# Kernel optimization log

Hardware: AMD Instinct MI355X
Metric: run time of the kernel (lower is better)

The kernel has to match this reference:

```python
import jax, jax.numpy as jnp
import numpy as np

NEG_INF = -1e30

def setup_inputs() -> dict:
    key0 = jax.random.key(0)
    kq, kk, kv, ks = jax.random.split(key0, 4)
    B, S, H, D = 4, 2048, 16, 128
    query = jax.random.normal(kq, (B, S, H, D), dtype=jnp.float32)
    key = jax.random.normal(kk, (B, S, H, D), dtype=jnp.float32)
    value = jax.random.normal(kv, (B, S, H, D), dtype=jnp.float32)
    decoder_segment_ids = jnp.sort(jax.random.randint(ks, (B, S), 0, 4), axis=-1).astype(jnp.int32)
    return {"query": query, "key": key, "value": value,
            "decoder_segment_ids": decoder_segment_ids}

def reference(query, key, value, decoder_segment_ids):
    # Splash causal attention, no 1/sqrt(d) scale (matches the wrapped kernel).
    B, S, H, D = query.shape
    # scores: [b, h, q, k]
    scores = jnp.einsum('bqhd,bkhd->bhqk', query, key)
    causal = jnp.tril(jnp.ones((S, S), dtype=bool))              # [q, k]
    seg = decoder_segment_ids
    seg_mask = seg[:, :, None] == seg[:, None, :]                # [b, q, k]
    mask = causal[None, None, :, :] & seg_mask[:, None, :, :]    # [b, 1->h, q, k]
    scores = jnp.where(mask, scores, NEG_INF)
    probs = jax.nn.softmax(scores, axis=-1)
    out = jnp.einsum('bhqk,bkhd->bqhd', probs, value)
    return out
```

## Files before the change

kernel.cpp:

```cpp
#include <hip/hip_runtime.h>
#include <hip/hip_bf16.h>

typedef short v8s __attribute__((ext_vector_type(8)));
typedef float f32x4 __attribute__((ext_vector_type(4)));

constexpr int Bb = 4, S = 2048, H = 16, Dd = 128;
constexpr int BQ = 64, BK = 32;
constexpr float NEG = -1e30f;

static __device__ inline short f2bs(float x) {
    __hip_bfloat16 h = __float2bfloat16(x);
    return *reinterpret_cast<short*>(&h);
}
static __device__ inline float bs2f(short s) {
    unsigned u = ((unsigned)(unsigned short)s) << 16;
    return __uint_as_float(u);
}

__global__ __launch_bounds__(256) void fa_fwd(const float* __restrict__ q,
                                              const float* __restrict__ k,
                                              const float* __restrict__ v,
                                              const int* __restrict__ seg,
                                              float* __restrict__ out) {
    __shared__ __align__(16) short Kh[BK][136];
    __shared__ __align__(16) short Kl[BK][136];
    __shared__ __align__(16) short Vt[Dd][40];
    __shared__ __align__(16) short Pl[4][16][40];

    const int qt = blockIdx.x, h = blockIdx.y, b = blockIdx.z;
    const int q0 = qt * BQ;
    const int tid = threadIdx.x;
    const int wave = tid >> 6, lane = tid & 63;
    const int quad = lane >> 4, l16 = lane & 15;

    const int rowA = q0 + wave * 16 + l16;
    const float* qbase = q + (((size_t)b * S + rowA) * H + h) * Dd;
    v8s qh[4], qlo[4];
#pragma unroll
    for (int c = 0; c < 4; ++c) {
        f32x4 x0 = *(const f32x4*)(qbase + c * 32 + quad * 8);
        f32x4 x1 = *(const f32x4*)(qbase + c * 32 + quad * 8 + 4);
#pragma unroll
        for (int i = 0; i < 4; ++i) {
            short h0 = f2bs(x0[i]); qh[c][i]     = h0; qlo[c][i]     = f2bs(x0[i] - bs2f(h0));
            short h1 = f2bs(x1[i]); qh[c][4 + i] = h1; qlo[c][4 + i] = f2bs(x1[i] - bs2f(h1));
        }
    }

    const int rowC0 = q0 + wave * 16 + quad * 4;
    int segq[4];
#pragma unroll
    for (int r = 0; r < 4; ++r) segq[r] = seg[b * S + rowC0 + r];
    const int seg_lo = seg[b * S + q0];

    f32x4 o[8];
#pragma unroll
    for (int dt = 0; dt < 8; ++dt) o[dt] = f32x4{0.f, 0.f, 0.f, 0.f};
    float m_i[4], l_i[4];
#pragma unroll
    for (int r = 0; r < 4; ++r) { m_i[r] = NEG; l_i[r] = 0.f; }

    const int nkt = (q0 + BQ) / BK;
    for (int it = 0; it < nkt; ++it) {
        const int kt = it * BK;
        if (seg[b * S + kt + BK - 1] < seg_lo) continue;

        {
            const int kk = tid >> 3, d0 = (tid & 7) * 16;
            const float* kb = k + (((size_t)b * S + kt + kk) * H + h) * Dd + d0;
            const float* vb = v + (((size_t)b * S + kt + kk) * H + h) * Dd + d0;
#pragma unroll
            for (int j = 0; j < 4; ++j) {
                f32x4 x = *(const f32x4*)(kb + j * 4);
#pragma unroll
                for (int i = 0; i < 4; ++i) {
                    short hb = f2bs(x[i]);
                    Kh[kk][d0 + j * 4 + i] = hb;
                    Kl[kk][d0 + j * 4 + i] = f2bs(x[i] - bs2f(hb));
                }
                f32x4 y = *(const f32x4*)(vb + j * 4);
#pragma unroll
                for (int i = 0; i < 4; ++i) Vt[d0 + j * 4 + i][kk] = f2bs(y[i]);
            }
        }
        __syncthreads();

        float sc[2][4];
#pragma unroll
        for (int nt = 0; nt < 2; ++nt) {
            f32x4 s = f32x4{0.f, 0.f, 0.f, 0.f};
#pragma unroll
            for (int c = 0; c < 4; ++c) {
                v8s kfh = *(const v8s*)&Kh[nt * 16 + l16][c * 32 + quad * 8];
                v8s kfl = *(const v8s*)&Kl[nt * 16 + l16][c * 32 + quad * 8];
                s = __builtin_amdgcn_mfma_f32_16x16x32_bf16(qh[c], kfh, s, 0, 0, 0);
                s = __builtin_amdgcn_mfma_f32_16x16x32_bf16(qlo[c], kfh, s, 0, 0, 0);
                s = __builtin_amdgcn_mfma_f32_16x16x32_bf16(qh[c], kfl, s, 0, 0, 0);
            }
            const int kj = kt + nt * 16 + l16;
            const int segk = seg[b * S + kj];
#pragma unroll
            for (int r = 0; r < 4; ++r) {
                const int qi = rowC0 + r;
                const bool valid = (kj <= qi) && (segk == segq[r]);
                sc[nt][r] = valid ? s[r] : NEG;
            }
        }

        float pr[2][4];
#pragma unroll
        for (int r = 0; r < 4; ++r) {
            float mx = fmaxf(sc[0][r], sc[1][r]);
#pragma unroll
            for (int off = 1; off < 16; off <<= 1) mx = fmaxf(mx, __shfl_xor(mx, off));
            const float mn = fmaxf(m_i[r], mx);
            const float alpha = __expf(m_i[r] - mn);
            const float p0 = (sc[0][r] <= 0.5f * NEG) ? 0.f : __expf(sc[0][r] - mn);
            const float p1 = (sc[1][r] <= 0.5f * NEG) ? 0.f : __expf(sc[1][r] - mn);
            float rs = p0 + p1;
#pragma unroll
            for (int off = 1; off < 16; off <<= 1) rs += __shfl_xor(rs, off);
            l_i[r] = l_i[r] * alpha + rs;
            m_i[r] = mn;
#pragma unroll
            for (int dt = 0; dt < 8; ++dt) o[dt][r] *= alpha;
            pr[0][r] = p0;
            pr[1][r] = p1;
        }

#pragma unroll
        for (int nt = 0; nt < 2; ++nt)
#pragma unroll
            for (int r = 0; r < 4; ++r)
                Pl[wave][quad * 4 + r][nt * 16 + l16] = f2bs(pr[nt][r]);
        __syncthreads();

        v8s pf = *(const v8s*)&Pl[wave][l16][quad * 8];
#pragma unroll
        for (int dt = 0; dt < 8; ++dt) {
            v8s vf = *(const v8s*)&Vt[dt * 16 + l16][quad * 8];
            o[dt] = __builtin_amdgcn_mfma_f32_16x16x32_bf16(pf, vf, o[dt], 0, 0, 0);
        }
        __syncthreads();
    }

    const size_t obase = (((size_t)b * S + rowC0) * H + h) * Dd;
#pragma unroll
    for (int r = 0; r < 4; ++r) {
        const float inv = 1.0f / l_i[r];
#pragma unroll
        for (int dt = 0; dt < 8; ++dt)
            out[obase + (size_t)r * H * Dd + dt * 16 + l16] = o[dt][r] * inv;
    }
}

extern "C" void kernel_launch(void* const* d_in, const int* in_sizes, int n_in,
                              void* d_out, int out_size, void* d_ws, size_t ws_size,
                              hipStream_t stream) {
    const float* q = (const float*)d_in[0];
    const float* k = (const float*)d_in[1];
    const float* v = (const float*)d_in[2];
    const int* seg = (const int*)d_in[3];
    float* out = (float*)d_out;
    dim3 grid(S / BQ, H, Bb);
    fa_fwd<<<grid, dim3(256), 0, stream>>>(q, k, v, seg, out);
}
```

Baseline: 403.9 us.

## Precompute bf16 hi/lo K and transposed V in workspace, prefetch tiles in register

Adds pre-pass kernels that split K into bf16 hi/lo halves and write a transposed bf16 V into workspace. The attention kernel then loads ready-made bf16 tiles with vector loads and register-prefetches the next non-skipped tile while computing the current one. It also drops a barrier between the per-wave P write and read. This removes repeated fp32 conversion and V transposition per query tile, at the cost of extra passes writing the converted K and V to memory. It falls back to the old kernel if the workspace is too small.

```diff
diff --git a/kernel.cpp b/kernel.cpp
--- a/kernel.cpp
+++ b/kernel.cpp
@@ -7,6 +7,7 @@
 constexpr int Bb = 4, S = 2048, H = 16, Dd = 128;
 constexpr int BQ = 64, BK = 32;
 constexpr float NEG = -1e30f;
+constexpr size_t NELEM = (size_t)Bb * S * H * Dd;
 
 static __device__ inline short f2bs(float x) {
     __hip_bfloat16 h = __float2bfloat16(x);
@@ -17,22 +18,212 @@
     return __uint_as_float(u);
 }
 
-__global__ __launch_bounds__(256) void fa_fwd(const float* __restrict__ q,
-                                              const float* __restrict__ k,
-                                              const float* __restrict__ v,
-                                              const int* __restrict__ seg,
-                                              float* __restrict__ out) {
+__global__ __launch_bounds__(256) void prep_k(const float* __restrict__ k,
+                                              short* __restrict__ khi,
+                                              short* __restrict__ klo) {
+    size_t i = ((size_t)blockIdx.x * 256 + threadIdx.x) * 8;
+    f32x4 a = *(const f32x4*)(k + i);
+    f32x4 b = *(const f32x4*)(k + i + 4);
+    v8s hi, lo;
+#pragma unroll
+    for (int j = 0; j < 4; ++j) {
+        short h0 = f2bs(a[j]); hi[j] = h0;     lo[j] = f2bs(a[j] - bs2f(h0));
+        short h1 = f2bs(b[j]); hi[4 + j] = h1; lo[4 + j] = f2bs(b[j] - bs2f(h1));
+    }
+    *(v8s*)(khi + i) = hi;
+    *(v8s*)(klo + i) = lo;
+}
+
+__global__ __launch_bounds__(256) void prep_vt(const float* __restrict__ v,
+                                               short* __restrict__ vt) {
+    __shared__ __align__(16) short T[64][136];
+    const int k0 = blockIdx.x * 64, h = blockIdx.y, b = blockIdx.z;
+    const int t = threadIdx.x;
+    {
+        const int kk = t >> 2, c0 = (t & 3) * 32;
+        const float* vb = v + (((size_t)b * S + k0 + kk) * H + h) * Dd + c0;
+        short tmp[32];
+#pragma unroll
+        for (int j = 0; j < 32; j += 4) {
+            f32x4 x = *(const f32x4*)(vb + j);
+#pragma unroll
+            for (int i = 0; i < 4; ++i) tmp[j + i] = f2bs(x[i]);
+        }
+#pragma unroll
+        for (int j = 0; j < 4; ++j) *(v8s*)&T[kk][c0 + j * 8] = *(v8s*)&tmp[j * 8];
+    }
+    __syncthreads();
+    {
+        const int d = t >> 1, koff = (t & 1) * 32;
+        short o16[32];
+#pragma unroll
+        for (int i = 0; i < 32; ++i) o16[i] = T[koff + i][d];
+        short* dst = vt + ((size_t)(b * H + h) * Dd + d) * S + k0 + koff;
+#pragma unroll
+        for (int j = 0; j < 4; ++j) *(v8s*)(dst + j * 8) = *(v8s*)&o16[j * 8];
+    }
+}
+
+__global__ __launch_bounds__(256) void fa_fast(const short* __restrict__ khi,
+                                               const short* __restrict__ klo,
+                                               const short* __restrict__ vtg,
+                                               const float* __restrict__ q,
+                                               const int* __restrict__ seg,
+                                               float* __restrict__ out) {
+    __shared__ __align__(16) short Khl[BK][136];
+    __shared__ __align__(16) short Kll[BK][136];
+    __shared__ __align__(16) short Vtl[Dd][40];
+    __shared__ __align__(16) short Pl[4][16][40];
+
+    const int qt = blockIdx.x, h = blockIdx.y, b = blockIdx.z;
+    const int q0 = qt * BQ, tid = threadIdx.x;
+    const int wave = tid >> 6, lane = tid & 63;
+    const int quad = lane >> 4, l16 = lane & 15;
+
+    const int rowA = q0 + wave * 16 + l16;
+    const float* qbase = q + (((size_t)b * S + rowA) * H + h) * Dd;
+    v8s qh[4], ql[4];
+#pragma unroll
+    for (int c = 0; c < 4; ++c) {
+        f32x4 x0 = *(const f32x4*)(qbase + c * 32 + quad * 8);
+        f32x4 x1 = *(const f32x4*)(qbase + c * 32 + quad * 8 + 4);
+#pragma unroll
+        for (int i = 0; i < 4; ++i) {
+            short h0 = f2bs(x0[i]); qh[c][i] = h0;     ql[c][i] = f2bs(x0[i] - bs2f(h0));
+            short h1 = f2bs(x1[i]); qh[c][4 + i] = h1; ql[c][4 + i] = f2bs(x1[i] - bs2f(h1));
+        }
+    }
+
+    const int rowC0 = q0 + wave * 16 + quad * 4;
+    const int segb = b * S;
+    int segq[4];
+#pragma unroll
+    for (int r = 0; r < 4; ++r) segq[r] = seg[segb + rowC0 + r];
+    const int seg_lo = seg[segb + q0];
+
+    f32x4 o[8];
+#pragma unroll
+    for (int dt = 0; dt < 8; ++dt) o[dt] = f32x4{0.f, 0.f, 0.f, 0.f};
+    float m_i[4], l_i[4];
+#pragma unroll
+    for (int r = 0; r < 4; ++r) { m_i[r] = NEG; l_i[r] = 0.f; }
+
+    const int skk = tid >> 3, scol = (tid & 7) * 16;
+    const int svd = tid >> 1, svo = (tid & 1) * 16;
+    const size_t kbase = (((size_t)b * S + skk) * H + h) * Dd + scol;
+    const size_t vbase = ((size_t)(b * H + h) * Dd + svd) * S + svo;
+
+    const int nkt = (q0 + BQ) / BK;
+    int it = 0;
+    while (it < nkt && seg[segb + it * BK + BK - 1] < seg_lo) ++it;
+
+    v8s pA, pB, pC, pD, pE, pF;
+    if (it < nkt) {
+        const size_t ka = kbase + (size_t)it * BK * H * Dd;
+        pA = *(const v8s*)(khi + ka); pB = *(const v8s*)(khi + ka + 8);
+        pC = *(const v8s*)(klo + ka); pD = *(const v8s*)(klo + ka + 8);
+        const size_t va = vbase + (size_t)it * BK;
+        pE = *(const v8s*)(vtg + va); pF = *(const v8s*)(vtg + va + 8);
+    }
+
+    while (it < nkt) {
+        *(v8s*)&Khl[skk][scol] = pA; *(v8s*)&Khl[skk][scol + 8] = pB;
+        *(v8s*)&Kll[skk][scol] = pC; *(v8s*)&Kll[skk][scol + 8] = pD;
+        *(v8s*)&Vtl[svd][svo]  = pE; *(v8s*)&Vtl[svd][svo + 8]  = pF;
+        __syncthreads();
+
+        const int kt = it * BK;
+        int nit = it + 1;
+        while (nit < nkt && seg[segb + nit * BK + BK - 1] < seg_lo) ++nit;
+        if (nit < nkt) {
+            const size_t ka = kbase + (size_t)nit * BK * H * Dd;
+            pA = *(const v8s*)(khi + ka); pB = *(const v8s*)(khi + ka + 8);
+            pC = *(const v8s*)(klo + ka); pD = *(const v8s*)(klo + ka + 8);
+            const size_t va = vbase + (size_t)nit * BK;
+            pE = *(const v8s*)(vtg + va); pF = *(const v8s*)(vtg + va + 8);
+        }
+
+        float sc_[2][4];
+#pragma unroll
+        for (int nt = 0; nt < 2; ++nt) {
+            f32x4 s = f32x4{0.f, 0.f, 0.f, 0.f};
+#pragma unroll
+            for (int c = 0; c < 4; ++c) {
+                v8s kfh = *(const v8s*)&Khl[nt * 16 + l16][c * 32 + quad * 8];
+                v8s kfl = *(const v8s*)&Kll[nt * 16 + l16][c * 32 + quad * 8];
+                s = __builtin_amdgcn_mfma_f32_16x16x32_bf16(qh[c], kfh, s, 0, 0, 0);
+                s = __builtin_amdgcn_mfma_f32_16x16x32_bf16(ql[c], kfh, s, 0, 0, 0);
+                s = __builtin_amdgcn_mfma_f32_16x16x32_bf16(qh[c], kfl, s, 0, 0, 0);
+            }
+            const int kj = kt + nt * 16 + l16;
+            const int sk = seg[segb + kj];
+#pragma unroll
+            for (int r = 0; r < 4; ++r) {
+                const bool valid = (kj <= rowC0 + r) && (sk == segq[r]);
+                sc_[nt][r] = valid ? s[r] : NEG;
+            }
+        }
+
+        float pr[2][4];
+#pragma unroll
+        for (int r = 0; r < 4; ++r) {
+            float mx = fmaxf(sc_[0][r], sc_[1][r]);
+#pragma unroll
+            for (int off = 1; off < 16; off <<= 1) mx = fmaxf(mx, __shfl_xor(mx, off));
+            const float mn = fmaxf(m_i[r], mx);
+            const float alpha = __expf(m_i[r] - mn);
+            const float p0 = (sc_[0][r] <= 0.5f * NEG) ? 0.f : __expf(sc_[0][r] - mn);
+            const float p1 = (sc_[1][r] <= 0.5f * NEG) ? 0.f : __expf(sc_[1][r] - mn);
+            float rs = p0 + p1;
+#pragma unroll
+            for (int off = 1; off < 16; off <<= 1) rs += __shfl_xor(rs, off);
+            l_i[r] = l_i[r] * alpha + rs;
+            m_i[r] = mn;
+#pragma unroll
+            for (int dt = 0; dt < 8; ++dt) o[dt][r] *= alpha;
+            pr[0][r] = p0;
+            pr[1][r] = p1;
+        }
+
+#pragma unroll
+        for (int nt = 0; nt < 2; ++nt)
+#pragma unroll
+            for (int r = 0; r < 4; ++r)
+                Pl[wave][quad * 4 + r][nt * 16 + l16] = f2bs(pr[nt][r]);
+
+        v8s pf = *(const v8s*)&Pl[wave][l16][quad * 8];
+#pragma unroll
+        for (int dt = 0; dt < 8; ++dt) {
+            v8s vf = *(const v8s*)&Vtl[dt * 16 + l16][quad * 8];
+            o[dt] = __builtin_amdgcn_mfma_f32_16x16x32_bf16(pf, vf, o[dt], 0, 0, 0);
+        }
+        __syncthreads();
+        it = nit;
+    }
+
+    const size_t obase = (((size_t)b * S + rowC0) * H + h) * Dd;
+#pragma unroll
+    for (int r = 0; r < 4; ++r) {
+        const float inv = 1.0f / l_i[r];
+#pragma unroll
+        for (int dt = 0; dt < 8; ++dt)
+            out[obase + (size_t)r * H * Dd + dt * 16 + l16] = o[dt][r] * inv;
+    }
+}
+
+__global__ __launch_bounds__(256) void fa_slow(const float* __restrict__ q,
+                                               const float* __restrict__ k,
+                                               const float* __restrict__ v,
+                                               const int* __restrict__ seg,
+                                               float* __restrict__ out) {
     __shared__ __align__(16) short Kh[BK][136];
     __shared__ __align__(16) short Kl[BK][136];
     __shared__ __align__(16) short Vt[Dd][40];
     __shared__ __align__(16) short Pl[4][16][40];
-
     const int qt = blockIdx.x, h = blockIdx.y, b = blockIdx.z;
-    const int q0 = qt * BQ;
-    const int tid = threadIdx.x;
+    const int q0 = qt * BQ, tid = threadIdx.x;
     const int wave = tid >> 6, lane = tid & 63;
     const int quad = lane >> 4, l16 = lane & 15;
-
     const int rowA = q0 + wave * 16 + l16;
     const float* qbase = q + (((size_t)b * S + rowA) * H + h) * Dd;
     v8s qh[4], qlo[4];
@@ -42,29 +233,25 @@
         f32x4 x1 = *(const f32x4*)(qbase + c * 32 + quad * 8 + 4);
 #pragma unroll
         for (int i = 0; i < 4; ++i) {
-            short h0 = f2bs(x0[i]); qh[c][i]     = h0; qlo[c][i]     = f2bs(x0[i] - bs2f(h0));
+            short h0 = f2bs(x0[i]); qh[c][i] = h0;     qlo[c][i] = f2bs(x0[i] - bs2f(h0));
             short h1 = f2bs(x1[i]); qh[c][4 + i] = h1; qlo[c][4 + i] = f2bs(x1[i] - bs2f(h1));
         }
     }
-
     const int rowC0 = q0 + wave * 16 + quad * 4;
     int segq[4];
 #pragma unroll
     for (int r = 0; r < 4; ++r) segq[r] = seg[b * S + rowC0 + r];
     const int seg_lo = seg[b * S + q0];
-
     f32x4 o[8];
 #pragma unroll
     for (int dt = 0; dt < 8; ++dt) o[dt] = f32x4{0.f, 0.f, 0.f, 0.f};
     float m_i[4], l_i[4];
 #pragma unroll
     for (int r = 0; r < 4; ++r) { m_i[r] = NEG; l_i[r] = 0.f; }
-
     const int nkt = (q0 + BQ) / BK;
-    for (int it = 0; it < nkt; ++it) {
-        const int kt = it * BK;
+    for (int itx = 0; itx < nkt; ++itx) {
+        const int kt = itx * BK;
         if (seg[b * S + kt + BK - 1] < seg_lo) continue;
-
         {
             const int kk = tid >> 3, d0 = (tid & 7) * 16;
             const float* kb = k + (((size_t)b * S + kt + kk) * H + h) * Dd + d0;
@@ -84,8 +271,7 @@
             }
         }
         __syncthreads();
-
-        float sc[2][4];
+        float sc_[2][4];
 #pragma unroll
         for (int nt = 0; nt < 2; ++nt) {
             f32x4 s = f32x4{0.f, 0.f, 0.f, 0.f};
@@ -101,22 +287,20 @@
             const int segk = seg[b * S + kj];
 #pragma unroll
             for (int r = 0; r < 4; ++r) {
-                const int qi = rowC0 + r;
-                const bool valid = (kj <= qi) && (segk == segq[r]);
-                sc[nt][r] = valid ? s[r] : NEG;
-            }
-        }
-
+                const bool valid = (kj <= rowC0 + r) && (segk == segq[r]);
+                sc_[nt][r] = valid ? s[r] : NEG;
+            }
+        }
         float pr[2][4];
 #pragma unroll
         for (int r = 0; r < 4; ++r) {
-            float mx = fmaxf(sc[0][r], sc[1][r]);
+            float mx = fmaxf(sc_[0][r], sc_[1][r]);
 #pragma unroll
             for (int off = 1; off < 16; off <<= 1) mx = fmaxf(mx, __shfl_xor(mx, off));
             const float mn = fmaxf(m_i[r], mx);
             const float alpha = __expf(m_i[r] - mn);
-            const float p0 = (sc[0][r] <= 0.5f * NEG) ? 0.f : __expf(sc[0][r] - mn);
-            const float p1 = (sc[1][r] <= 0.5f * NEG) ? 0.f : __expf(sc[1][r] - mn);
+            const float p0 = (sc_[0][r] <= 0.5f * NEG) ? 0.f : __expf(sc_[0][r] - mn);
+            const float p1 = (sc_[1][r] <= 0.5f * NEG) ? 0.f : __expf(sc_[1][r] - mn);
             float rs = p0 + p1;
 #pragma unroll
             for (int off = 1; off < 16; off <<= 1) rs += __shfl_xor(rs, off);
@@ -127,14 +311,11 @@
             pr[0][r] = p0;
             pr[1][r] = p1;
         }
-
 #pragma unroll
         for (int nt = 0; nt < 2; ++nt)
 #pragma unroll
             for (int r = 0; r < 4; ++r)
                 Pl[wave][quad * 4 + r][nt * 16 + l16] = f2bs(pr[nt][r]);
-        __syncthreads();
-
         v8s pf = *(const v8s*)&Pl[wave][l16][quad * 8];
 #pragma unroll
         for (int dt = 0; dt < 8; ++dt) {
@@ -143,7 +324,6 @@
         }
         __syncthreads();
     }
-
     const size_t obase = (((size_t)b * S + rowC0) * H + h) * Dd;
 #pragma unroll
     for (int r = 0; r < 4; ++r) {
@@ -162,6 +342,16 @@
     const float* v = (const float*)d_in[2];
     const int* seg = (const int*)d_in[3];
     float* out = (float*)d_out;
+    const size_t need = NELEM * 2 * 3;
     dim3 grid(S / BQ, H, Bb);
-    fa_fwd<<<grid, dim3(256), 0, stream>>>(q, k, v, seg, out);
-}
+    if (ws_size >= need) {
+        short* khi = (short*)d_ws;
+        short* klo = khi + NELEM;
+        short* vtg = klo + NELEM;
+        prep_k<<<(int)(NELEM / (256 * 8)), 256, 0, stream>>>(k, khi, klo);
+        prep_vt<<<dim3(S / 64, H, Bb), 256, 0, stream>>>(v, vtg);
+        fa_fast<<<grid, dim3(256), 0, stream>>>(khi, klo, vtg, q, seg, out);
+    } else {
+        fa_slow<<<grid, dim3(256), 0, stream>>>(q, k, v, seg, out);
+    }
+}
```

Result: faster. 395.0 us (-2.2%).
